# Optimization experiments

Hardware: AMD Instinct MI355X
Metric: run time of the kernel (lower is better)

Reference implementation:

```python
import jax, jax.numpy as jnp
import numpy as np

D_MODEL = 1024
NUM_HEADS = 16


def setup_inputs() -> dict:
    key = jax.random.key(0)
    ks = jax.random.split(key, 5)
    B, T, d = 2, 2048, D_MODEL
    s = 1.0 / np.sqrt(d)
    return {
        "x": jax.random.normal(ks[0], (B, T, d), dtype=jnp.float32),
        "W_kqv": jax.random.normal(ks[1], (d, 3 * d), dtype=jnp.float32) * s,
        "b_kqv": jax.random.normal(ks[2], (3 * d,), dtype=jnp.float32) * 0.02,
        "W_o": jax.random.normal(ks[3], (d, d), dtype=jnp.float32) * s,
        "b_o": jax.random.normal(ks[4], (d,), dtype=jnp.float32) * 0.02,
    }


def reference(x, W_kqv, b_kqv, W_o, b_o):
    B, T, d = x.shape
    H = NUM_HEADS
    dk = d // H
    kqv = x @ W_kqv + b_kqv                      # [B, T, 3d]
    # source splits as contiguous chunks in order K, Q, V
    K, Q, V = jnp.split(kqv, 3, axis=-1)
    # [B, T, d] -> [B, H, T, dk]
    to_heads = lambda t: t.reshape(B, T, H, dk).transpose(0, 2, 1, 3)
    K, Q, V = to_heads(K), to_heads(Q), to_heads(V)
    scores = jnp.einsum("bhtd,bhsd->bhts", Q, K)  # [B, H, T, T]
    causal = jnp.triu(jnp.ones((T, T), dtype=bool), k=1)
    scores = jnp.where(causal, -jnp.inf, scores)
    attn = jax.nn.softmax(scores / jnp.sqrt(jnp.asarray(dk, x.dtype)), axis=-1)
    out = jnp.einsum("bhts,bhsd->bhtd", attn, V)  # [B, H, T, dk]
    out = out.transpose(0, 2, 1, 3).reshape(B, T, d)
    return out @ W_o + b_o
```

## Files before the change

### kernel.cpp

```cpp
#include <hip/hip_runtime.h>
#include <hip/hip_bf16.h>
#include <stdint.h>
#include <math.h>

using bf16x8 = __attribute__((ext_vector_type(8))) short;
using f32x4  = __attribute__((ext_vector_type(4))) float;
using f32x16 = __attribute__((ext_vector_type(16))) float;

#define NHEAD  16
#define DK     64
#define TSEQ   2048
#define DMODEL 1024
#define MTOT   4096

#define QSCALE 0.18033688011112042f

static __device__ __forceinline__ ushort f2bf(float f) {
  union { float f; uint32_t u; } v; v.f = f;
  return (ushort)((v.u + 0x7FFFu + ((v.u >> 16) & 1u)) >> 16);
}

static __device__ __forceinline__ float bf2f(ushort u) {
  union { uint32_t u; float f; } v; v.u = ((uint32_t)u) << 16;
  return v.f;
}

static __device__ __forceinline__ uint32_t cvtpk_bf16(float lo, float hi) {
  uint32_t r;
  asm("v_cvt_pk_bf16_f32 %0, %1, %2" : "=v"(r) : "v"(lo), "v"(hi));
  return r;
}

static __device__ __forceinline__ void gload_lds16(const ushort* g, ushort* l) {
  typedef __attribute__((address_space(1))) const uint32_t gu32;
  typedef __attribute__((address_space(3))) uint32_t lu32;
  __builtin_amdgcn_global_load_lds((gu32*)g, (lu32*)l, 16, 0, 0);
}

__global__ void cvt_bf16_kernel(const float* __restrict__ in, ushort* __restrict__ out, int n) {
  int i = (blockIdx.x * 256 + threadIdx.x) * 8;
  const int stride = gridDim.x * 256 * 8;
  for (; i < n; i += stride) {
    const float4* p = (const float4*)(in + i);
    float4 a = p[0], b = p[1];
    bf16x8 v;
    v[0]=(short)f2bf(a.x); v[1]=(short)f2bf(a.y); v[2]=(short)f2bf(a.z); v[3]=(short)f2bf(a.w);
    v[4]=(short)f2bf(b.x); v[5]=(short)f2bf(b.y); v[6]=(short)f2bf(b.z); v[7]=(short)f2bf(b.w);
    *(bf16x8*)(out + i) = v;
  }
}

__global__ __launch_bounds__(256) void transpose_cvt_kernel(const float* __restrict__ W,
                                                            ushort* __restrict__ Wt, int K, int N) {
  __shared__ ushort tl[64][66];
  const int n0 = blockIdx.x * 64, k0 = blockIdx.y * 64;
  const int c = threadIdx.x & 63, r0 = threadIdx.x >> 6;
#pragma unroll
  for (int i = 0; i < 64; i += 4)
    tl[i + r0][c] = f2bf(W[(size_t)(k0 + i + r0) * N + n0 + c]);
  __syncthreads();
#pragma unroll
  for (int i = 0; i < 64; i += 4)
    Wt[(size_t)(n0 + i + r0) * K + k0 + c] = tl[c][i + r0];
}

__global__ __launch_bounds__(256) void transpose_v_kernel(const ushort* __restrict__ V,
                                                          ushort* __restrict__ Vt) {
  __shared__ ushort tl[64][66];
  const int bh = blockIdx.y, t0 = blockIdx.x * 64;
  const int c = threadIdx.x & 63, r0 = threadIdx.x >> 6;
  const ushort* Vb = V + (size_t)bh * TSEQ * DK;
  ushort* Vtb = Vt + (size_t)bh * DK * TSEQ;
#pragma unroll
  for (int i = 0; i < 64; i += 4)
    tl[i + r0][c] = Vb[(size_t)(t0 + i + r0) * DK + c];
  __syncthreads();
#pragma unroll
  for (int i = 0; i < 64; i += 4)
    Vtb[(size_t)(i + r0) * TSEQ + t0 + c] = tl[c][i + r0];
}

template <int MODE>
__global__ __launch_bounds__(256, 3)
void gemm_bt_kernel(const ushort* __restrict__ A, const ushort* __restrict__ Bt,
                    const float* __restrict__ bias,
                    ushort* __restrict__ oK, ushort* __restrict__ oQ, ushort* __restrict__ oV,
                    float* __restrict__ oF, int N, int K) {
  __shared__ ushort As[128 * 32];
  __shared__ ushort Bs[128 * 32];
  const int tid = threadIdx.x;
  const int w = tid >> 6, lane = tid & 63;
  const int m0 = blockIdx.y * 128, n0 = blockIdx.x * 128;
  const int wr = (w >> 1) * 64, wc = (w & 1) * 64;

  const int e0 = ((w * 2 + 0) * 64 + lane) * 8;
  const int e1 = ((w * 2 + 1) * 64 + lane) * 8;
  const ushort* pA0 = A  + (size_t)(m0 + (e0 >> 5)) * K + (e0 & 31);
  const ushort* pA1 = A  + (size_t)(m0 + (e1 >> 5)) * K + (e1 & 31);
  const ushort* pB0 = Bt + (size_t)(n0 + (e0 >> 5)) * K + (e0 & 31);
  const ushort* pB1 = Bt + (size_t)(n0 + (e1 >> 5)) * K + (e1 & 31);

  f32x4 acc[4][4];
#pragma unroll
  for (int i = 0; i < 4; i++)
#pragma unroll
    for (int j = 0; j < 4; j++) acc[i][j] = (f32x4){0.f, 0.f, 0.f, 0.f};

  const int aro = (wr + (lane & 15)) * 32 + (lane >> 4) * 8;
  const int bro = (wc + (lane & 15)) * 32 + (lane >> 4) * 8;

  for (int k0 = 0; k0 < K; k0 += 32) {
    __syncthreads();
    gload_lds16(pA0 + k0, &As[e0]);
    gload_lds16(pA1 + k0, &As[e1]);
    gload_lds16(pB0 + k0, &Bs[e0]);
    gload_lds16(pB1 + k0, &Bs[e1]);
    __syncthreads();
    bf16x8 af[4], bfr[4];
#pragma unroll
    for (int i = 0; i < 4; i++) af[i]  = *(const bf16x8*)&As[aro + i * 16 * 32];
#pragma unroll
    for (int j = 0; j < 4; j++) bfr[j] = *(const bf16x8*)&Bs[bro + j * 16 * 32];
#pragma unroll
    for (int i = 0; i < 4; i++)
#pragma unroll
      for (int j = 0; j < 4; j++)
        acc[i][j] = __builtin_amdgcn_mfma_f32_16x16x32_bf16(af[i], bfr[j], acc[i][j], 0, 0, 0);
  }

  const int rbase = m0 + wr + (lane >> 4) * 4;
  const int cbase = n0 + wc + (lane & 15);
#pragma unroll
  for (int i = 0; i < 4; i++) {
#pragma unroll
    for (int j = 0; j < 4; j++) {
      const int gn = cbase + j * 16;
      const float bv = bias[gn];
#pragma unroll
      for (int jj = 0; jj < 4; jj++) {
        const int gm = rbase + i * 16 + jj;
        float val = acc[i][j][jj] + bv;
        if (MODE == 0) {
          const int sel = gn >> 10, cc = gn & 1023;
          const int hh = cc >> 6, dd = cc & 63;
          const int bbx = gm >> 11, t = gm & 2047;
          if (sel == 1) val *= QSCALE;
          ushort* dst = (sel == 0) ? oK : (sel == 1) ? oQ : oV;
          dst[((size_t)((bbx * NHEAD + hh) * TSEQ + t)) * DK + dd] = f2bf(val);
        } else {
          oF[(size_t)gm * N + gn] = val;
        }
      }
    }
  }
}

__global__ __launch_bounds__(256, 4)
void attn_kernel(const ushort* __restrict__ Qb, const ushort* __restrict__ Kb,
                 const ushort* __restrict__ Vtb, ushort* __restrict__ Opart,
                 float2* __restrict__ mlbuf) {
  __shared__ ushort Ks[2][64 * 64];
  __shared__ ushort Vs[2][64 * 64];

  const int bid = blockIdx.x;
  const int xcd = bid & 7, i = bid >> 3;
  const int bh = xcd + 8 * (i / 40);
  const int jj = 39 - (i % 40);
  int qi, p;
  if (jj < 4)       { qi = jj;                 p = 0; }
  else if (jj < 12) { int t = jj - 4;  qi = 4  + (t >> 1); p = t & 1; }
  else if (jj < 24) { int t = jj - 12; qi = 8  + t / 3;    p = t % 3; }
  else              { int t = jj - 24; qi = 12 + (t >> 2); p = t & 3; }

  const int q0 = qi * 128;
  const int tid = threadIdx.x, w = tid >> 6, lane = tid & 63;
  const int l31 = lane & 31, h = lane >> 5;
  const int qrow = q0 + w * 32 + l31;

  const int t_begin = p * 8;
  const int ntp = min(t_begin + 8, 2 * qi + 2) - t_begin;

  const ushort* Qp = Qb + ((size_t)bh * TSEQ + qrow) * DK;
  bf16x8 qf[4];
#pragma unroll
  for (int c = 0; c < 4; c++)
    qf[c] = *(const bf16x8*)(Qp + c * 16 + h * 8);

  f32x16 oacc0, oacc1;
#pragma unroll
  for (int r = 0; r < 16; r++) { oacc0[r] = 0.f; oacc1[r] = 0.f; }
  float mrun = -INFINITY, lrun = 0.f;

  const int Bl0 = w * 128 + lane, Bl1 = Bl0 + 64;
  const int sr0 = Bl0 >> 3, sc0 = ((Bl0 & 7) ^ (sr0 & 7)) * 8;
  const int sr1 = Bl1 >> 3, sc1 = ((Bl1 & 7) ^ (sr1 & 7)) * 8;
  const ushort* Kp0 = Kb  + (size_t)bh * TSEQ * DK + sr0 * DK + sc0;
  const ushort* Kp1 = Kb  + (size_t)bh * TSEQ * DK + sr1 * DK + sc1;
  const ushort* Vp0 = Vtb + (size_t)bh * DK * TSEQ + sr0 * TSEQ + sc0;
  const ushort* Vp1 = Vtb + (size_t)bh * DK * TSEQ + sr1 * TSEQ + sc1;

  {
    const int s0 = t_begin * 64;
    gload_lds16(Kp0 + s0 * DK, &Ks[0][Bl0 * 8]);
    gload_lds16(Kp1 + s0 * DK, &Ks[0][Bl1 * 8]);
    gload_lds16(Vp0 + s0, &Vs[0][Bl0 * 8]);
    gload_lds16(Vp1 + s0, &Vs[0][Bl1 * 8]);
  }
  asm volatile("s_waitcnt vmcnt(0)" ::: "memory");
  __builtin_amdgcn_s_barrier();

  for (int tt = 0; tt < ntp; tt++) {
    const int s0 = (t_begin + tt) * 64, cur = tt & 1;

    if (tt + 1 < ntp) {
      const int sn = (t_begin + tt + 1) * 64, nb = cur ^ 1;
      gload_lds16(Kp0 + sn * DK, &Ks[nb][Bl0 * 8]);
      gload_lds16(Kp1 + sn * DK, &Ks[nb][Bl1 * 8]);
      gload_lds16(Vp0 + sn, &Vs[nb][Bl0 * 8]);
      gload_lds16(Vp1 + sn, &Vs[nb][Bl1 * 8]);
    }

    const bool active = (s0 <= q0 + w * 32 + 31);
    if (active) {
      f32x16 ps0, ps1;
#pragma unroll
      for (int r = 0; r < 16; r++) { ps0[r] = 0.f; ps1[r] = 0.f; }
      const char* Kbase = (const char*)&Ks[cur][0];
      __builtin_amdgcn_s_setprio(1);
#pragma unroll
      for (int c = 0; c < 4; c++) {
        const int r0 = l31, r1 = 32 + l31;
        bf16x8 kf0 = *(const bf16x8*)(Kbase + r0 * 128 + ((c * 32 + h * 16) ^ ((r0 & 7) << 4)));
        bf16x8 kf1 = *(const bf16x8*)(Kbase + r1 * 128 + ((c * 32 + h * 16) ^ ((r1 & 7) << 4)));
        ps0 = __builtin_amdgcn_mfma_f32_32x32x16_bf16(kf0, qf[c], ps0, 0, 0, 0);
        ps1 = __builtin_amdgcn_mfma_f32_32x32x16_bf16(kf1, qf[c], ps1, 0, 0, 0);
      }
      __builtin_amdgcn_s_setprio(0);

      if (s0 + 63 > q0 + w * 32) {
#pragma unroll
        for (int r = 0; r < 16; r++) {
          const int kv0 = s0 + (r & 3) + 8 * (r >> 2) + 4 * h;
          if (kv0 > qrow)      ps0[r] = -INFINITY;
          if (kv0 + 32 > qrow) ps1[r] = -INFINITY;
        }
      }

      float pm = ps0[0];
#pragma unroll
      for (int r = 1; r < 16; r++) pm = fmaxf(pm, ps0[r]);
#pragma unroll
      for (int r = 0; r < 16; r++) pm = fmaxf(pm, ps1[r]);
      pm = fmaxf(pm, __shfl_xor(pm, 32));

      if (!__all(pm <= mrun + 8.0f)) {
        const float nm = fmaxf(mrun, pm);
        const float scl = exp2f(mrun - nm);
        lrun *= scl;
#pragma unroll
        for (int r = 0; r < 16; r++) { oacc0[r] *= scl; oacc1[r] *= scl; }
        mrun = nm;
      }

#pragma unroll
      for (int r = 0; r < 16; r++) ps0[r] = exp2f(ps0[r] - mrun);
#pragma unroll
      for (int r = 0; r < 16; r++) ps1[r] = exp2f(ps1[r] - mrun);
      float rs = 0.f;
#pragma unroll
      for (int r = 0; r < 16; r++) rs += ps0[r] + ps1[r];
      rs += __shfl_xor(rs, 32);
      lrun += rs;

      uint32_t w0[2][4], w1[2][4];
#pragma unroll
      for (int a = 0; a < 4; a++) {
        w0[0][a] = cvtpk_bf16(ps0[4 * a + 0], ps0[4 * a + 1]);
        w1[0][a] = cvtpk_bf16(ps0[4 * a + 2], ps0[4 * a + 3]);
        w0[1][a] = cvtpk_bf16(ps1[4 * a + 0], ps1[4 * a + 1]);
        w1[1][a] = cvtpk_bf16(ps1[4 * a + 2], ps1[4 * a + 3]);
      }

      const char* Vbase = (const char*)&Vs[cur][0];
#pragma unroll
      for (int s = 0; s < 2; s++) {
#pragma unroll
        for (int u = 0; u < 2; u++) {
          const int t = 2 * s + u;
          const uint32_t sw0 = h ? w0[s][2 * u] : w0[s][2 * u + 1];
          const uint32_t sw1 = h ? w1[s][2 * u] : w1[s][2 * u + 1];
          const uint32_t rx0 = (uint32_t)__shfl_xor((int)sw0, 32);
          const uint32_t rx1 = (uint32_t)__shfl_xor((int)sw1, 32);
          int4 pw;
          pw.x = h ? (int)rx0 : (int)w0[s][2 * u];
          pw.y = h ? (int)rx1 : (int)w1[s][2 * u];
          pw.z = h ? (int)w0[s][2 * u + 1] : (int)rx0;
          pw.w = h ? (int)w1[s][2 * u + 1] : (int)rx1;
          const bf16x8 pf = __builtin_bit_cast(bf16x8, pw);

          const int vr0 = l31, vr1 = 32 + l31;
          bf16x8 vf0 = *(const bf16x8*)(Vbase + vr0 * 128 + ((t * 32 + h * 16) ^ ((vr0 & 7) << 4)));
          bf16x8 vf1 = *(const bf16x8*)(Vbase + vr1 * 128 + ((t * 32 + h * 16) ^ ((vr1 & 7) << 4)));
          __builtin_amdgcn_s_setprio(1);
          oacc0 = __builtin_amdgcn_mfma_f32_32x32x16_bf16(vf0, pf, oacc0, 0, 0, 0);
          oacc1 = __builtin_amdgcn_mfma_f32_32x32x16_bf16(vf1, pf, oacc1, 0, 0, 0);
          __builtin_amdgcn_s_setprio(0);
        }
      }
    }

    asm volatile("s_waitcnt vmcnt(0)" ::: "memory");
    __builtin_amdgcn_s_barrier();
  }

  const int partIdx = (bh * 16 + qi) * 4 + p;
  const size_t rowslot = (size_t)partIdx * 128 + (qrow & 127);
  ushort* orow = Opart + rowslot * 64;
#pragma unroll
  for (int r = 0; r < 16; r += 2) {
    const int d0 = (r & 3) + 8 * (r >> 2) + 4 * h;
    const uint32_t v0 = (uint32_t)f2bf(oacc0[r]) | ((uint32_t)f2bf(oacc0[r + 1]) << 16);
    const uint32_t v1 = (uint32_t)f2bf(oacc1[r]) | ((uint32_t)f2bf(oacc1[r + 1]) << 16);
    *(uint32_t*)(orow + d0)      = v0;
    *(uint32_t*)(orow + 32 + d0) = v1;
  }
  if (h == 0) mlbuf[rowslot] = make_float2(mrun, lrun);
}

__global__ __launch_bounds__(256) void combine_kernel(const ushort* __restrict__ Opart,
                                                      const float2* __restrict__ mlbuf,
                                                      ushort* __restrict__ AO) {
  const int gid = blockIdx.x * 4 + (threadIdx.x >> 6);
  const int lane = threadIdx.x & 63;
  const int bh = gid >> 11, q = gid & 2047;
  const int qi = q >> 7, np = (qi >> 2) + 1;
  const size_t base = ((size_t)(bh * 16 + qi) * 4) * 128 + (q & 127);

  float M = -INFINITY;
  for (int p = 0; p < np; p++) M = fmaxf(M, mlbuf[base + (size_t)p * 128].x);
  float den = 0.f, acc = 0.f;
  for (int p = 0; p < np; p++) {
    const float2 ml = mlbuf[base + (size_t)p * 128];
    const float wp = exp2f(ml.x - M);
    den += wp * ml.y;
    acc += wp * bf2f(Opart[(base + (size_t)p * 128) * 64 + lane]);
  }
  const float val = acc / den;
  const int bb = bh >> 4, hd = bh & 15;
  AO[((size_t)bb * TSEQ + q) * DMODEL + hd * DK + lane] = f2bf(val);
}

extern "C" void kernel_launch(void* const* d_in, const int* in_sizes, int n_in,
                              void* d_out, int out_size, void* d_ws, size_t ws_size,
                              hipStream_t stream) {
  (void)in_sizes; (void)n_in; (void)out_size; (void)ws_size;
  const float* x    = (const float*)d_in[0];
  const float* Wkqv = (const float*)d_in[1];
  const float* bkqv = (const float*)d_in[2];
  const float* Wo   = (const float*)d_in[3];
  const float* bo   = (const float*)d_in[4];
  float* out = (float*)d_out;

  char* ws = (char*)d_ws;
  const size_t MB = 1024 * 1024;
  ushort* x_bf   = (ushort*)(ws + 0);
  ushort* wkqv_t = (ushort*)(ws + 8 * MB);
  ushort* wo_t   = (ushort*)(ws + 14 * MB);
  ushort* Kbuf   = (ushort*)(ws + 16 * MB);
  ushort* Qbuf   = (ushort*)(ws + 24 * MB);
  ushort* Vbuf   = (ushort*)(ws + 32 * MB);
  ushort* Vtbuf  = (ushort*)(ws + 40 * MB);
  ushort* AObuf  = (ushort*)(ws + 48 * MB);
  ushort* Opart  = (ushort*)(ws + 56 * MB);
  float2* mlbuf  = (float2*)(ws + 88 * MB);

  cvt_bf16_kernel<<<2048, 256, 0, stream>>>(x, x_bf, MTOT * DMODEL);
  transpose_cvt_kernel<<<dim3(3072 / 64, 1024 / 64), 256, 0, stream>>>(Wkqv, wkqv_t, 1024, 3072);
  transpose_cvt_kernel<<<dim3(1024 / 64, 1024 / 64), 256, 0, stream>>>(Wo, wo_t, 1024, 1024);
  gemm_bt_kernel<0><<<dim3(3072 / 128, 4096 / 128), 256, 0, stream>>>(
      x_bf, wkqv_t, bkqv, Kbuf, Qbuf, Vbuf, nullptr, 3072, 1024);
  transpose_v_kernel<<<dim3(TSEQ / 64, 32), 256, 0, stream>>>(Vbuf, Vtbuf);
  attn_kernel<<<1280, 256, 0, stream>>>(Qbuf, Kbuf, Vtbuf, Opart, mlbuf);
  combine_kernel<<<16384, 256, 0, stream>>>(Opart, mlbuf, AObuf);
  gemm_bt_kernel<1><<<dim3(1024 / 128, 4096 / 128), 256, 0, stream>>>(
      AObuf, wo_t, bo, nullptr, nullptr, nullptr, out, 1024, 1024);
}
```

Measured before the change: 215.5 us.

## Double-buffer GEMM LDS loads, merge weight transposes, raise attention occupancy

The GEMM main loop now double-buffers its LDS tiles, prefetching the next K slice while the MFMAs run on the current one, and raises wave priority around the MFMA block. This replaces two barriers per iteration with one. The two weight transpose-convert launches are merged into a single launch, and the attention kernel's launch bounds are raised to request 5 blocks per SM. The cost is twice the GEMM LDS footprint and register pressure in attention, which may spill.

Result: slower. 229.0 us (+6.2%).

```diff
diff --git a/kernel.cpp b/kernel.cpp
--- a/kernel.cpp
+++ b/kernel.cpp
@@ -50,10 +50,16 @@
   }
 }
 
-__global__ __launch_bounds__(256) void transpose_cvt_kernel(const float* __restrict__ W,
-                                                            ushort* __restrict__ Wt, int K, int N) {
+__global__ __launch_bounds__(256) void transpose_cvt2_kernel(const float* __restrict__ W1,
+                                                             ushort* __restrict__ Wt1,
+                                                             const float* __restrict__ W2,
+                                                             ushort* __restrict__ Wt2) {
   __shared__ ushort tl[64][66];
-  const int n0 = blockIdx.x * 64, k0 = blockIdx.y * 64;
+  const int bx = blockIdx.x;
+  const float* W; ushort* Wt; int N, n0;
+  if (bx < 48) { W = W1; Wt = Wt1; N = 3072; n0 = bx * 64; }
+  else         { W = W2; Wt = Wt2; N = 1024; n0 = (bx - 48) * 64; }
+  const int k0 = blockIdx.y * 64;
   const int c = threadIdx.x & 63, r0 = threadIdx.x >> 6;
 #pragma unroll
   for (int i = 0; i < 64; i += 4)
@@ -61,7 +67,7 @@
   __syncthreads();
 #pragma unroll
   for (int i = 0; i < 64; i += 4)
-    Wt[(size_t)(n0 + i + r0) * K + k0 + c] = tl[c][i + r0];
+    Wt[(size_t)(n0 + i + r0) * 1024 + k0 + c] = tl[c][i + r0];
 }
 
 __global__ __launch_bounds__(256) void transpose_v_kernel(const ushort* __restrict__ V,
@@ -86,8 +92,8 @@
                     const float* __restrict__ bias,
                     ushort* __restrict__ oK, ushort* __restrict__ oQ, ushort* __restrict__ oV,
                     float* __restrict__ oF, int N, int K) {
-  __shared__ ushort As[128 * 32];
-  __shared__ ushort Bs[128 * 32];
+  __shared__ ushort As[2][128 * 32];
+  __shared__ ushort Bs[2][128 * 32];
   const int tid = threadIdx.x;
   const int w = tid >> 6, lane = tid & 63;
   const int m0 = blockIdx.y * 128, n0 = blockIdx.x * 128;
@@ -109,23 +115,36 @@
   const int aro = (wr + (lane & 15)) * 32 + (lane >> 4) * 8;
   const int bro = (wc + (lane & 15)) * 32 + (lane >> 4) * 8;
 
+  gload_lds16(pA0, &As[0][e0]);
+  gload_lds16(pA1, &As[0][e1]);
+  gload_lds16(pB0, &Bs[0][e0]);
+  gload_lds16(pB1, &Bs[0][e1]);
+  asm volatile("s_waitcnt vmcnt(0)" ::: "memory");
+  __builtin_amdgcn_s_barrier();
+
   for (int k0 = 0; k0 < K; k0 += 32) {
-    __syncthreads();
-    gload_lds16(pA0 + k0, &As[e0]);
-    gload_lds16(pA1 + k0, &As[e1]);
-    gload_lds16(pB0 + k0, &Bs[e0]);
-    gload_lds16(pB1 + k0, &Bs[e1]);
-    __syncthreads();
+    const int cur = (k0 >> 5) & 1;
+    if (k0 + 32 < K) {
+      const int nb = cur ^ 1, kn = k0 + 32;
+      gload_lds16(pA0 + kn, &As[nb][e0]);
+      gload_lds16(pA1 + kn, &As[nb][e1]);
+      gload_lds16(pB0 + kn, &Bs[nb][e0]);
+      gload_lds16(pB1 + kn, &Bs[nb][e1]);
+    }
     bf16x8 af[4], bfr[4];
 #pragma unroll
-    for (int i = 0; i < 4; i++) af[i]  = *(const bf16x8*)&As[aro + i * 16 * 32];
-#pragma unroll
-    for (int j = 0; j < 4; j++) bfr[j] = *(const bf16x8*)&Bs[bro + j * 16 * 32];
+    for (int i = 0; i < 4; i++) af[i]  = *(const bf16x8*)&As[cur][aro + i * 16 * 32];
+#pragma unroll
+    for (int j = 0; j < 4; j++) bfr[j] = *(const bf16x8*)&Bs[cur][bro + j * 16 * 32];
+    __builtin_amdgcn_s_setprio(1);
 #pragma unroll
     for (int i = 0; i < 4; i++)
 #pragma unroll
       for (int j = 0; j < 4; j++)
         acc[i][j] = __builtin_amdgcn_mfma_f32_16x16x32_bf16(af[i], bfr[j], acc[i][j], 0, 0, 0);
+    __builtin_amdgcn_s_setprio(0);
+    asm volatile("s_waitcnt vmcnt(0)" ::: "memory");
+    __builtin_amdgcn_s_barrier();
   }
 
   const int rbase = m0 + wr + (lane >> 4) * 4;
@@ -155,7 +174,7 @@
   }
 }
 
-__global__ __launch_bounds__(256, 4)
+__global__ __launch_bounds__(256, 5)
 void attn_kernel(const ushort* __restrict__ Qb, const ushort* __restrict__ Kb,
                  const ushort* __restrict__ Vtb, ushort* __restrict__ Opart,
                  float2* __restrict__ mlbuf) {
@@ -375,8 +394,7 @@
   float2* mlbuf  = (float2*)(ws + 88 * MB);
 
   cvt_bf16_kernel<<<2048, 256, 0, stream>>>(x, x_bf, MTOT * DMODEL);
-  transpose_cvt_kernel<<<dim3(3072 / 64, 1024 / 64), 256, 0, stream>>>(Wkqv, wkqv_t, 1024, 3072);
-  transpose_cvt_kernel<<<dim3(1024 / 64, 1024 / 64), 256, 0, stream>>>(Wo, wo_t, 1024, 1024);
+  transpose_cvt2_kernel<<<dim3(64, 16), 256, 0, stream>>>(Wkqv, wkqv_t, Wo, wo_t);
   gemm_bt_kernel<0><<<dim3(3072 / 128, 4096 / 128), 256, 0, stream>>>(
       x_bf, wkqv_t, bkqv, Kbuf, Qbuf, Vbuf, nullptr, 3072, 1024);
   transpose_v_kernel<<<dim3(TSEQ / 64, 32), 256, 0, stream>>>(Vbuf, Vtbuf);
```
